# Performance work log

Measured on AMD Instinct MI355X. Metric: run time of the kernel, lower is better.

## Reference

```python
import jax, jax.numpy as jnp
import numpy as np

L_, H_, D_, GRP_ = 16, 16, 64, 4  # num_layers, num_heads, dims, conv groups factor


def setup_inputs() -> dict:
    key = jax.random.key(0)
    k1, k2, k3 = jax.random.split(key, 3)
    B, K, n, E = 4, 4, 256, 768
    G = GRP_ * L_ * 2                      # 128 conv groups
    Cin_g = E * L_ * 2 // G                # 192 in-channels per group
    Cout_g = H_ * D_ * L_ * 2 // G         # 256 out-channels per group
    rng = np.random.default_rng(0)
    lengths = rng.integers(n // 2, n + 1, size=B * K)
    mask = (np.arange(n)[None, :] < lengths[:, None]).astype(np.int32)
    last_hidden = jax.random.normal(k1, (B * K, n, E), jnp.float32) * 0.02
    weight = jax.random.normal(k2, (G, Cout_g, Cin_g), jnp.float32) * 0.02
    bias = jax.random.normal(k3, (G * Cout_g,), jnp.float32) * 0.02
    return {"last_hidden": last_hidden, "attention_mask": jnp.asarray(mask),
            "weight": weight, "bias": bias, "k": K}


def _forward(last_hidden, weight, bias, mask_np, k):
    Bk, n, E = last_hidden.shape
    B = Bk // k
    G = weight.shape[0]
    # mean pooling over valid tokens
    mask_f = jnp.asarray(mask_np).astype(last_hidden.dtype)
    pooled = (last_hidden * mask_f[..., None]).sum(1) / mask_f.sum(1)[..., None]
    # tile along feature dim (L*2 copies), move channels first: [Bk, E*2L, n]
    x = jnp.tile(last_hidden, (1, 1, 2 * L_)).transpose(0, 2, 1)
    x = x.reshape(Bk, G, -1, n)  # [Bk, G, Cin/G, n]
    # grouped 1x1 conv == per-group GEMM
    y = jnp.einsum('bgin,goi->bgon', x, weight).reshape(Bk, -1, n) + bias[None, :, None]
    # [B, k, L, 2, D, H, n] -> permute(0,1,2,3,5,6,4) -> [B, k, L, 2, H, n, D]
    y = y.reshape(B, k, L_, 2, D_, H_, n).transpose(0, 1, 2, 3, 5, 6, 4)
    # bring (k, n) together for ragged gather: [B, k*n, L, 2, H, D]
    y = y.transpose(0, 1, 5, 2, 3, 4, 6).reshape(B, k * n, L_, 2, H_, D_)
    lens = mask_np.sum(1).reshape(B, k)
    Tmax = int(lens.sum(1).max())
    idx = np.zeros((B, Tmax), np.int32)
    valid = np.zeros((B, Tmax), np.int32)
    for i in range(B):  # tiny host-side loop over B to build gather map
        pos = np.concatenate([j * n + np.arange(lens[i, j]) for j in range(k)])
        idx[i, :pos.size] = pos
        valid[i, :pos.size] = 1
    batch = y[jnp.arange(B)[:, None], jnp.asarray(idx)]  # [B, Tmax, L, 2, H, D]
    batch = batch * jnp.asarray(valid)[:, :, None, None, None, None].astype(batch.dtype)
    batch = batch.transpose(2, 3, 0, 4, 1, 5)  # [L, 2, B, H, Tmax, D]
    return pooled, batch, jnp.asarray(valid, jnp.int32)


def reference(last_hidden, attention_mask, weight, bias, k):
    mask_np = np.asarray(attention_mask)
    return _forward(last_hidden, weight, bias, mask_np, k)
```

## Files before the change

kernel.cpp:

```cpp
#include <hip/hip_runtime.h>
#include <hip/hip_bf16.h>


typedef float f32x4 __attribute__((ext_vector_type(4)));
typedef __bf16 bf16x8 __attribute__((ext_vector_type(8)));
typedef unsigned short u16x4 __attribute__((ext_vector_type(4)));
typedef unsigned short u16x8 __attribute__((ext_vector_type(8)));

__device__ __forceinline__ unsigned short f2bf(float f) {
    union { float f; unsigned u; } v; v.f = f;
    unsigned r = v.u + 0x7FFFu + ((v.u >> 16) & 1u);
    return (unsigned short)(r >> 16);
}

__device__ __forceinline__ bf16x8 ldfrag(const unsigned short* p) {
    u16x8 r = *(const u16x8*)p;
    return __builtin_bit_cast(bf16x8, r);
}

__global__ void cums_kernel(const int* __restrict__ mask, int* __restrict__ ws,
                            float* __restrict__ valid_out, int Tmax) {
    int tid = threadIdx.x;
    int w = tid >> 6, lane = tid & 63;
    int m = mask[w * 256 + lane] + mask[w * 256 + lane + 64] +
            mask[w * 256 + lane + 128] + mask[w * 256 + lane + 192];
#pragma unroll
    for (int off = 32; off > 0; off >>= 1) m += __shfl_down(m, off);
    if (lane == 0) ws[w] = m;
    __syncthreads();
    if (tid == 0) {
        for (int b = 0; b < 4; ++b) {
            int c = 0;
            for (int j = 0; j < 4; ++j) { ws[16 + b * 4 + j] = c; c += ws[b * 4 + j]; }
            ws[32 + b] = c;
        }
    }
    __syncthreads();
    for (int i = tid; i < 4 * Tmax; i += 1024) {
        int b = i / Tmax;
        int T = i - b * Tmax;
        valid_out[i] = (T < ws[32 + b]) ? 1.0f : 0.0f;
    }
}

__global__ void pooled_kernel(const float* __restrict__ lh, const int* __restrict__ mask,
                              const int* __restrict__ ws, float* __restrict__ pooled) {
    int bs = blockIdx.x / 12;
    int ec = blockIdx.x - bs * 12;
    int tid = threadIdx.x;
    int tg = tid >> 6, lane = tid & 63;
    int e = ec * 64 + lane;
    float s = 0.f;
    for (int t = tg; t < 256; t += 4) {
        float mf = (float)mask[bs * 256 + t];
        s += lh[(size_t)(bs * 256 + t) * 768 + e] * mf;
    }
    __shared__ float red[4][64];
    red[tg][lane] = s;
    __syncthreads();
    if (tg == 0) {
        float tot = red[0][lane] + red[1][lane] + red[2][lane] + red[3][lane];
        pooled[bs * 768 + e] = tot / (float)ws[bs];
    }
}

__global__ void zerotail_kernel(float* __restrict__ batch, const int* __restrict__ ws,
                                int Tmax) {
    int rr = blockIdx.x;
    int b = rr >> 9;
    int rem = rr & 511;
    int l = rem >> 5, s = (rem >> 4) & 1, h = rem & 15;
    int total = ws[32 + b];
    int span = Tmax - total;
    if (span <= 0) return;
    float* row = batch + (((size_t)((l * 2 + s) * 4 + b) * 16 + h) * (size_t)Tmax + total) * 64;
    f32x4 z = {0.f, 0.f, 0.f, 0.f};
    int nchunk = span << 4;
    for (int j = threadIdx.x; j < nchunk; j += 256)
        *(f32x4*)(row + (j << 2)) = z;
}

__global__ void packw_kernel(const float* __restrict__ wgt, unsigned short* __restrict__ Wp) {
    int bid = blockIdx.x;
    int ls = bid / 96;
    int rem = bid - ls * 96;
    int kk = rem >> 4;
    int blk = rem & 15;
    int slot = (blk << 8) + threadIdx.x;
    int row = slot >> 2;
    int sc = slot & 3;
    int coloff = (sc ^ ((row >> 1) & 3)) << 3;
    const float* src = wgt + (size_t)ls * 196608 + row * 192 + (kk << 5) + coloff;
    f32x4 a0 = *(const f32x4*)src;
    f32x4 a1 = *(const f32x4*)(src + 4);
    u16x8 w = { f2bf(a0[0]), f2bf(a0[1]), f2bf(a0[2]), f2bf(a0[3]),
                f2bf(a1[0]), f2bf(a1[1]), f2bf(a1[2]), f2bf(a1[3]) };
    *(u16x8*)(Wp + (((size_t)(ls * 6 + kk) << 12) + slot) * 8) = w;
}

__global__ void packlh_kernel(const float* __restrict__ lh, unsigned short* __restrict__ Lp) {
    size_t slot = (size_t)blockIdx.x * 256 + threadIdx.x;
    const float* src = lh + slot * 8;
    f32x4 a0 = *(const f32x4*)src;
    f32x4 a1 = *(const f32x4*)(src + 4);
    u16x8 w = { f2bf(a0[0]), f2bf(a0[1]), f2bf(a0[2]), f2bf(a0[3]),
                f2bf(a1[0]), f2bf(a1[1]), f2bf(a1[2]), f2bf(a1[3]) };
    *(u16x8*)(Lp + slot * 8) = w;
}

template<bool PACKED>
__global__ __launch_bounds__(512, 4) void gemm_kernel(
    const float* __restrict__ lh, const float* __restrict__ wgt,
    const unsigned short* __restrict__ Wp, const unsigned short* __restrict__ Lp,
    const float* __restrict__ bias, const int* __restrict__ ws,
    float* __restrict__ out, int Tmax) {
    __shared__ __align__(16) unsigned short As[1024][32];
    __shared__ __align__(16) float biasT[16][68];

    int x = blockIdx.x;
    int xcd = x & 7;
    int rest = x >> 3;
    int lsq = rest >> 7;
    int rb = rest & 127;
    int ls = (lsq << 3) + xcd;
    int bs = rb >> 3;
    int tq = rb & 7;

    int len = ws[bs];
    int tbase = tq << 5;
    if (tbase >= len) return;

    int tid = threadIdx.x;

    {
        int i0 = tid, i1 = tid + 512;
        biasT[i0 & 15][((i0 >> 8) << 4) + ((i0 & 255) >> 4)] = bias[(ls << 10) + i0];
        biasT[i1 & 15][((i1 >> 8) << 4) + ((i1 & 255) >> 4)] = bias[(ls << 10) + i1];
    }

    int lane = tid & 63;
    int wv = tid >> 6;
    int beta = wv >> 1, oh = wv & 1;
    int p = lane & 15, q = lane >> 4;

    f32x4 acc[8][2] = {};

#pragma unroll
    for (int cc = 0; cc < 6; ++cc) {
        const int kk = cc << 5;
        if constexpr (PACKED) {
            const char* gbase = (const char*)Wp +
                (((size_t)(ls * 6 + cc) << 12) + (wv << 6) + lane) * 16;
            char* lbase = ((char*)&As[0][0]) + ((wv << 6) << 4);
#pragma unroll
            for (int it = 0; it < 8; ++it)
                __builtin_amdgcn_global_load_lds(
                    (const __attribute__((address_space(1))) void*)(gbase + it * 8192),
                    (__attribute__((address_space(3))) void*)(lbase + it * 8192), 16, 0, 0);
        } else {
            const float* Awg = wgt + (size_t)ls * 196608;
            int arow0 = tid >> 2;
            int achk = tid & 3;
#pragma unroll
            for (int it = 0; it < 8; ++it) {
                int row = arow0 + (it << 7);
                const float* src = Awg + row * 192 + kk + (achk << 3);
                f32x4 a0 = *(const f32x4*)src;
                f32x4 a1 = *(const f32x4*)(src + 4);
                u16x8 aw = { f2bf(a0[0]), f2bf(a0[1]), f2bf(a0[2]), f2bf(a0[3]),
                             f2bf(a1[0]), f2bf(a1[1]), f2bf(a1[2]), f2bf(a1[3]) };
                *(u16x8*)&As[row][(achk ^ ((row >> 1) & 3)) << 3] = aw;
            }
        }
        bf16x8 bf[2];
        if constexpr (PACKED) {
            const unsigned short* Brow = Lp + ((size_t)(bs * 256 + tbase + p)) * 768 +
                                         beta * 192 + (q << 3) + kk;
            bf[0] = ldfrag(Brow);
            bf[1] = ldfrag(Brow + 16 * 768);
        } else {
            const float* Brow = lh + (size_t)bs * 196608 + (size_t)(tbase + p) * 768 +
                                beta * 192 + (q << 3) + kk;
#pragma unroll
            for (int n = 0; n < 2; ++n) {
                const float* bp = Brow + n * 16 * 768;
                f32x4 b0 = *(const f32x4*)bp;
                f32x4 b1 = *(const f32x4*)(bp + 4);
                u16x8 bw = { f2bf(b0[0]), f2bf(b0[1]), f2bf(b0[2]), f2bf(b0[3]),
                             f2bf(b1[0]), f2bf(b1[1]), f2bf(b1[2]), f2bf(b1[3]) };
                bf[n] = __builtin_bit_cast(bf16x8, bw);
            }
        }
        __syncthreads();
#pragma unroll
        for (int r8 = 0; r8 < 8; ++r8) {
            int row = (beta << 8) + (oh << 7) + (r8 << 4) + p;
            bf16x8 af = ldfrag(&As[row][(q ^ ((row >> 1) & 3)) << 3]);
            acc[r8][0] = __builtin_amdgcn_mfma_f32_16x16x32_bf16(af, bf[0], acc[r8][0], 0, 0, 0);
            acc[r8][1] = __builtin_amdgcn_mfma_f32_16x16x32_bf16(af, bf[1], acc[r8][1], 0, 0, 0);
        }
        __syncthreads();
    }

    float* Ltr = (float*)&As[0][0];
    int cum = ws[16 + bs];
    int b = bs >> 2;
    float* batch = out + 12288;
    size_t hd0 = (size_t)((ls << 2) + b) << 4;

    int toff = lane & 3, dcq = lane >> 2;
    int col0 = (beta << 4) + (oh << 3);

#pragma unroll
    for (int r = 0; r < 4; ++r) {
#pragma unroll
        for (int n = 0; n < 2; ++n) {
            int rowL = (((n << 4) + p) << 2) + q;
            f32x4 v0 = { acc[0][n][r], acc[1][n][r], acc[2][n][r], acc[3][n][r] };
            f32x4 v1 = { acc[4][n][r], acc[5][n][r], acc[6][n][r], acc[7][n][r] };
            *(f32x4*)(Ltr + rowL * 68 + col0) = v0;
            *(f32x4*)(Ltr + rowL * 68 + col0 + 4) = v1;
        }
        __syncthreads();
#pragma unroll
        for (int gi = 0; gi < 4; ++gi) {
            int flat = (wv << 2) + gi;
            int hq = flat >> 3, t4 = flat & 7;
            int tloc = (t4 << 2) + toff;
            int h = (hq << 2) + r;
            int tglob = tbase + tloc;
            f32x4 v = *(const f32x4*)(Ltr + ((tloc << 2) + hq) * 68 + (dcq << 2));
            v += *(const f32x4*)&biasT[h][dcq << 2];
            if (tglob < len) {
                float* dst = batch + ((hd0 + h) * (size_t)Tmax + cum + tglob) * 64;
                *(f32x4*)(dst + (dcq << 2)) = v;
            }
        }
        __syncthreads();
    }
}

extern "C" void kernel_launch(void* const* d_in, const int* in_sizes, int n_in,
                              void* d_out, int out_size, void* d_ws, size_t ws_size,
                              hipStream_t stream) {
    const float* lh   = (const float*)d_in[0];
    const int*   mask = (const int*)d_in[1];
    const float* wgt  = (const float*)d_in[2];
    const float* bias = (const float*)d_in[3];
    float* out = (float*)d_out;
    int* ws = (int*)d_ws;

    int Tmax = (out_size - 12288) / 131076;

    unsigned short* Wp = (unsigned short*)((char*)d_ws + 1024);
    unsigned short* Lp = (unsigned short*)((char*)d_ws + 1024 + 12582912);
    const size_t need = 1024 + 12582912 + 6291456;
    bool packed = ws_size >= need;

    cums_kernel<<<1, 1024, 0, stream>>>(mask, ws, out + 12288 + (size_t)131072 * Tmax, Tmax);
    pooled_kernel<<<16 * 12, 256, 0, stream>>>(lh, mask, ws, out);
    zerotail_kernel<<<2048, 256, 0, stream>>>(out + 12288, ws, Tmax);

    if (packed) {
        packw_kernel<<<3072, 256, 0, stream>>>(wgt, Wp);
        packlh_kernel<<<1536, 256, 0, stream>>>(lh, Lp);
        gemm_kernel<true><<<4096, 512, 0, stream>>>(lh, wgt, Wp, Lp, bias, ws, out, Tmax);
    } else {
        gemm_kernel<false><<<4096, 512, 0, stream>>>(lh, wgt, Wp, Lp, bias, ws, out, Tmax);
    }
}
```

Measured before the change: 228.9 us.

## Warp-specialize GEMM into producer/consumer halves and fuse bf16 packing into pooling

The packed GEMM now splits its eight waves into two groups that take turns. In each half-phase one group runs MFMAs at raised priority while the other issues the next K-chunk's global-to-LDS weight loads and activation fragment loads, so memory latency overlaps with compute. Separately, the bf16 conversion of the activations moves into the pooling kernel, which already reads them, removing the separate packlh launch and its extra pass over the input. In exchange, each wave does only half the MFMA issue per phase, and the pooling kernel's bf16 stores are scalar 2-byte writes that may coalesce poorly.

```diff
diff --git a/kernel.cpp b/kernel.cpp
--- a/kernel.cpp
+++ b/kernel.cpp
@@ -44,7 +44,8 @@
 }
 
 __global__ void pooled_kernel(const float* __restrict__ lh, const int* __restrict__ mask,
-                              const int* __restrict__ ws, float* __restrict__ pooled) {
+                              const int* __restrict__ ws, float* __restrict__ pooled,
+                              unsigned short* __restrict__ Lp) {
     int bs = blockIdx.x / 12;
     int ec = blockIdx.x - bs * 12;
     int tid = threadIdx.x;
@@ -52,8 +53,10 @@
     int e = ec * 64 + lane;
     float s = 0.f;
     for (int t = tg; t < 256; t += 4) {
-        float mf = (float)mask[bs * 256 + t];
-        s += lh[(size_t)(bs * 256 + t) * 768 + e] * mf;
+        size_t off = (size_t)(bs * 256 + t) * 768 + e;
+        float v = lh[off];
+        if (Lp) Lp[off] = f2bf(v);
+        s += v * (float)mask[bs * 256 + t];
     }
     __shared__ float red[4][64];
     red[tg][lane] = s;
@@ -98,19 +101,7 @@
     *(u16x8*)(Wp + (((size_t)(ls * 6 + kk) << 12) + slot) * 8) = w;
 }
 
-__global__ void packlh_kernel(const float* __restrict__ lh, unsigned short* __restrict__ Lp) {
-    size_t slot = (size_t)blockIdx.x * 256 + threadIdx.x;
-    const float* src = lh + slot * 8;
-    f32x4 a0 = *(const f32x4*)src;
-    f32x4 a1 = *(const f32x4*)(src + 4);
-    u16x8 w = { f2bf(a0[0]), f2bf(a0[1]), f2bf(a0[2]), f2bf(a0[3]),
-                f2bf(a1[0]), f2bf(a1[1]), f2bf(a1[2]), f2bf(a1[3]) };
-    *(u16x8*)(Lp + slot * 8) = w;
-}
-
-template<bool PACKED>
-__global__ __launch_bounds__(512, 4) void gemm_kernel(
-    const float* __restrict__ lh, const float* __restrict__ wgt,
+__global__ __launch_bounds__(512, 4) void gemm_pc(
     const unsigned short* __restrict__ Wp, const unsigned short* __restrict__ Lp,
     const float* __restrict__ bias, const int* __restrict__ ws,
     float* __restrict__ out, int Tmax) {
@@ -141,63 +132,58 @@
     int lane = tid & 63;
     int wv = tid >> 6;
     int beta = wv >> 1, oh = wv & 1;
+    int grp = wv >> 2;
     int p = lane & 15, q = lane >> 4;
 
+    const unsigned short* BrowU = Lp + ((size_t)(bs * 256 + tbase + p)) * 768 +
+                                  beta * 192 + (q << 3);
+    const char* WpB = (const char*)Wp;
+    char* AsB = (char*)&As[0][0];
+
     f32x4 acc[8][2] = {};
-
-#pragma unroll
-    for (int cc = 0; cc < 6; ++cc) {
-        const int kk = cc << 5;
-        if constexpr (PACKED) {
-            const char* gbase = (const char*)Wp +
-                (((size_t)(ls * 6 + cc) << 12) + (wv << 6) + lane) * 16;
-            char* lbase = ((char*)&As[0][0]) + ((wv << 6) << 4);
-#pragma unroll
-            for (int it = 0; it < 8; ++it)
-                __builtin_amdgcn_global_load_lds(
-                    (const __attribute__((address_space(1))) void*)(gbase + it * 8192),
-                    (__attribute__((address_space(3))) void*)(lbase + it * 8192), 16, 0, 0);
+    bf16x8 bfn[2];
+
+    {
+        const char* g0 = WpB + ((size_t)(ls * 6) << 16) + (tid << 4);
+        char* l0 = AsB + (wv << 10);
+#pragma unroll
+        for (int it = 0; it < 4; ++it)
+            __builtin_amdgcn_global_load_lds(
+                (const __attribute__((address_space(1))) void*)(g0 + it * 8192),
+                (__attribute__((address_space(3))) void*)(l0 + it * 8192), 16, 0, 0);
+        if (grp == 0) {
+            bfn[0] = ldfrag(BrowU);
+            bfn[1] = ldfrag(BrowU + 12288);
+        }
+    }
+    __syncthreads();
+
+    for (int ph = 0; ph < 12; ++ph) {
+        int cc = ph >> 1, sub = ph & 1;
+        if (grp == sub) {
+            __builtin_amdgcn_s_setprio(1);
+#pragma unroll
+            for (int r8 = 0; r8 < 8; ++r8) {
+                int row = (beta << 8) + (oh << 7) + (r8 << 4) + p;
+                bf16x8 af = ldfrag(&As[row][(q ^ ((row >> 1) & 3)) << 3]);
+                acc[r8][0] = __builtin_amdgcn_mfma_f32_16x16x32_bf16(af, bfn[0], acc[r8][0], 0, 0, 0);
+                acc[r8][1] = __builtin_amdgcn_mfma_f32_16x16x32_bf16(af, bfn[1], acc[r8][1], 0, 0, 0);
+            }
+            __builtin_amdgcn_s_setprio(0);
         } else {
-            const float* Awg = wgt + (size_t)ls * 196608;
-            int arow0 = tid >> 2;
-            int achk = tid & 3;
-#pragma unroll
-            for (int it = 0; it < 8; ++it) {
-                int row = arow0 + (it << 7);
-                const float* src = Awg + row * 192 + kk + (achk << 3);
-                f32x4 a0 = *(const f32x4*)src;
-                f32x4 a1 = *(const f32x4*)(src + 4);
-                u16x8 aw = { f2bf(a0[0]), f2bf(a0[1]), f2bf(a0[2]), f2bf(a0[3]),
-                             f2bf(a1[0]), f2bf(a1[1]), f2bf(a1[2]), f2bf(a1[3]) };
-                *(u16x8*)&As[row][(achk ^ ((row >> 1) & 3)) << 3] = aw;
+            int scc = cc + sub;
+            if (scc < 6) {
+                const char* g = WpB + (((size_t)(ls * 6 + scc)) << 16) +
+                                (grp << 15) + ((wv & 3) << 10) + (lane << 4);
+                char* l = AsB + (grp << 15) + ((wv & 3) << 10);
+#pragma unroll
+                for (int it = 0; it < 8; ++it)
+                    __builtin_amdgcn_global_load_lds(
+                        (const __attribute__((address_space(1))) void*)(g + it * 4096),
+                        (__attribute__((address_space(3))) void*)(l + it * 4096), 16, 0, 0);
+                bfn[0] = ldfrag(BrowU + (scc << 5));
+                bfn[1] = ldfrag(BrowU + 12288 + (scc << 5));
             }
-        }
-        bf16x8 bf[2];
-        if constexpr (PACKED) {
-            const unsigned short* Brow = Lp + ((size_t)(bs * 256 + tbase + p)) * 768 +
-                                         beta * 192 + (q << 3) + kk;
-            bf[0] = ldfrag(Brow);
-            bf[1] = ldfrag(Brow + 16 * 768);
-        } else {
-            const float* Brow = lh + (size_t)bs * 196608 + (size_t)(tbase + p) * 768 +
-                                beta * 192 + (q << 3) + kk;
-#pragma unroll
-            for (int n = 0; n < 2; ++n) {
-                const float* bp = Brow + n * 16 * 768;
-                f32x4 b0 = *(const f32x4*)bp;
-                f32x4 b1 = *(const f32x4*)(bp + 4);
-                u16x8 bw = { f2bf(b0[0]), f2bf(b0[1]), f2bf(b0[2]), f2bf(b0[3]),
-                             f2bf(b1[0]), f2bf(b1[1]), f2bf(b1[2]), f2bf(b1[3]) };
-                bf[n] = __builtin_bit_cast(bf16x8, bw);
-            }
-        }
-        __syncthreads();
-#pragma unroll
-        for (int r8 = 0; r8 < 8; ++r8) {
-            int row = (beta << 8) + (oh << 7) + (r8 << 4) + p;
-            bf16x8 af = ldfrag(&As[row][(q ^ ((row >> 1) & 3)) << 3]);
-            acc[r8][0] = __builtin_amdgcn_mfma_f32_16x16x32_bf16(af, bf[0], acc[r8][0], 0, 0, 0);
-            acc[r8][1] = __builtin_amdgcn_mfma_f32_16x16x32_bf16(af, bf[1], acc[r8][1], 0, 0, 0);
         }
         __syncthreads();
     }
@@ -240,6 +226,117 @@
     }
 }
 
+__global__ __launch_bounds__(512, 4) void gemm_fb(
+    const float* __restrict__ lh, const float* __restrict__ wgt,
+    const float* __restrict__ bias, const int* __restrict__ ws,
+    float* __restrict__ out, int Tmax) {
+    __shared__ __align__(16) unsigned short As[1024][32];
+    __shared__ __align__(16) float biasT[16][68];
+
+    int x = blockIdx.x;
+    int xcd = x & 7;
+    int rest = x >> 3;
+    int lsq = rest >> 7;
+    int rb = rest & 127;
+    int ls = (lsq << 3) + xcd;
+    int bs = rb >> 3;
+    int tq = rb & 7;
+
+    int len = ws[bs];
+    int tbase = tq << 5;
+    if (tbase >= len) return;
+
+    int tid = threadIdx.x;
+    {
+        int i0 = tid, i1 = tid + 512;
+        biasT[i0 & 15][((i0 >> 8) << 4) + ((i0 & 255) >> 4)] = bias[(ls << 10) + i0];
+        biasT[i1 & 15][((i1 >> 8) << 4) + ((i1 & 255) >> 4)] = bias[(ls << 10) + i1];
+    }
+
+    int lane = tid & 63;
+    int wv = tid >> 6;
+    int beta = wv >> 1, oh = wv & 1;
+    int p = lane & 15, q = lane >> 4;
+
+    f32x4 acc[8][2] = {};
+
+#pragma unroll
+    for (int cc = 0; cc < 6; ++cc) {
+        const int kk = cc << 5;
+        const float* Awg = wgt + (size_t)ls * 196608;
+        int arow0 = tid >> 2;
+        int achk = tid & 3;
+#pragma unroll
+        for (int it = 0; it < 8; ++it) {
+            int row = arow0 + (it << 7);
+            const float* src = Awg + row * 192 + kk + (achk << 3);
+            f32x4 a0 = *(const f32x4*)src;
+            f32x4 a1 = *(const f32x4*)(src + 4);
+            u16x8 aw = { f2bf(a0[0]), f2bf(a0[1]), f2bf(a0[2]), f2bf(a0[3]),
+                         f2bf(a1[0]), f2bf(a1[1]), f2bf(a1[2]), f2bf(a1[3]) };
+            *(u16x8*)&As[row][(achk ^ ((row >> 1) & 3)) << 3] = aw;
+        }
+        bf16x8 bf[2];
+        const float* Brow = lh + (size_t)bs * 196608 + (size_t)(tbase + p) * 768 +
+                            beta * 192 + (q << 3) + kk;
+#pragma unroll
+        for (int n = 0; n < 2; ++n) {
+            const float* bp = Brow + n * 16 * 768;
+            f32x4 b0 = *(const f32x4*)bp;
+            f32x4 b1 = *(const f32x4*)(bp + 4);
+            u16x8 bw = { f2bf(b0[0]), f2bf(b0[1]), f2bf(b0[2]), f2bf(b0[3]),
+                         f2bf(b1[0]), f2bf(b1[1]), f2bf(b1[2]), f2bf(b1[3]) };
+            bf[n] = __builtin_bit_cast(bf16x8, bw);
+        }
+        __syncthreads();
+#pragma unroll
+        for (int r8 = 0; r8 < 8; ++r8) {
+            int row = (beta << 8) + (oh << 7) + (r8 << 4) + p;
+            bf16x8 af = ldfrag(&As[row][(q ^ ((row >> 1) & 3)) << 3]);
+            acc[r8][0] = __builtin_amdgcn_mfma_f32_16x16x32_bf16(af, bf[0], acc[r8][0], 0, 0, 0);
+            acc[r8][1] = __builtin_amdgcn_mfma_f32_16x16x32_bf16(af, bf[1], acc[r8][1], 0, 0, 0);
+        }
+        __syncthreads();
+    }
+
+    float* Ltr = (float*)&As[0][0];
+    int cum = ws[16 + bs];
+    int b = bs >> 2;
+    float* batch = out + 12288;
+    size_t hd0 = (size_t)((ls << 2) + b) << 4;
+
+    int toff = lane & 3, dcq = lane >> 2;
+    int col0 = (beta << 4) + (oh << 3);
+
+#pragma unroll
+    for (int r = 0; r < 4; ++r) {
+#pragma unroll
+        for (int n = 0; n < 2; ++n) {
+            int rowL = (((n << 4) + p) << 2) + q;
+            f32x4 v0 = { acc[0][n][r], acc[1][n][r], acc[2][n][r], acc[3][n][r] };
+            f32x4 v1 = { acc[4][n][r], acc[5][n][r], acc[6][n][r], acc[7][n][r] };
+            *(f32x4*)(Ltr + rowL * 68 + col0) = v0;
+            *(f32x4*)(Ltr + rowL * 68 + col0 + 4) = v1;
+        }
+        __syncthreads();
+#pragma unroll
+        for (int gi = 0; gi < 4; ++gi) {
+            int flat = (wv << 2) + gi;
+            int hq = flat >> 3, t4 = flat & 7;
+            int tloc = (t4 << 2) + toff;
+            int h = (hq << 2) + r;
+            int tglob = tbase + tloc;
+            f32x4 v = *(const f32x4*)(Ltr + ((tloc << 2) + hq) * 68 + (dcq << 2));
+            v += *(const f32x4*)&biasT[h][dcq << 2];
+            if (tglob < len) {
+                float* dst = batch + ((hd0 + h) * (size_t)Tmax + cum + tglob) * 64;
+                *(f32x4*)(dst + (dcq << 2)) = v;
+            }
+        }
+        __syncthreads();
+    }
+}
+
 extern "C" void kernel_launch(void* const* d_in, const int* in_sizes, int n_in,
                               void* d_out, int out_size, void* d_ws, size_t ws_size,
                               hipStream_t stream) {
@@ -258,14 +355,13 @@
     bool packed = ws_size >= need;
 
     cums_kernel<<<1, 1024, 0, stream>>>(mask, ws, out + 12288 + (size_t)131072 * Tmax, Tmax);
-    pooled_kernel<<<16 * 12, 256, 0, stream>>>(lh, mask, ws, out);
+    pooled_kernel<<<16 * 12, 256, 0, stream>>>(lh, mask, ws, out, packed ? Lp : nullptr);
     zerotail_kernel<<<2048, 256, 0, stream>>>(out + 12288, ws, Tmax);
 
     if (packed) {
         packw_kernel<<<3072, 256, 0, stream>>>(wgt, Wp);
-        packlh_kernel<<<1536, 256, 0, stream>>>(lh, Lp);
-        gemm_kernel<true><<<4096, 512, 0, stream>>>(lh, wgt, Wp, Lp, bias, ws, out, Tmax);
+        gemm_pc<<<4096, 512, 0, stream>>>(Wp, Lp, bias, ws, out, Tmax);
     } else {
-        gemm_kernel<false><<<4096, 512, 0, stream>>>(lh, wgt, Wp, Lp, bias, ws, out, Tmax);
-    }
-}
+        gemm_fb<<<4096, 512, 0, stream>>>(lh, wgt, bias, ws, out, Tmax);
+    }
+}
```

Measured after the change: 248.5 us. 1.09x slower.
